# Kernel tuning notes

Measured on AMD Instinct MI355X. Metric: run time of the kernel, lower is better.

Reference implementation:

```python
import jax, jax.numpy as jnp
import numpy as np

VOXEL = 0.1      # voxel_size[0] == voxel_size[1]
OUT_FACTOR = 8
PC_MIN = -51.2   # pc_range[0] == pc_range[1]
OVERLAP = 0.2    # gaussian_overlap
MIN_RADIUS = 2
FH = FW = 128    # 1024 // 8


def gaussian_radius(height, width, min_overlap):
    # mmdet3d / CenterPoint formula, vectorized; returns min(r1, r2, r3)
    b1 = height + width
    c1 = width * height * (1.0 - min_overlap) / (1.0 + min_overlap)
    sq1 = jnp.sqrt(jnp.maximum(b1 * b1 - 4.0 * c1, 0.0))
    r1 = (b1 + sq1) / 2.0

    b2 = 2.0 * (height + width)
    c2 = (1.0 - min_overlap) * width * height
    sq2 = jnp.sqrt(jnp.maximum(b2 * b2 - 16.0 * c2, 0.0))
    r2 = (b2 + sq2) / 2.0

    a3 = 4.0 * min_overlap
    b3 = -2.0 * min_overlap * (height + width)
    c3 = (min_overlap - 1.0) * width * height
    sq3 = jnp.sqrt(jnp.maximum(b3 * b3 - 4.0 * a3 * c3, 0.0))
    r3 = (b3 + sq3) / 2.0
    return jnp.minimum(jnp.minimum(r1, r2), r3)


def setup_inputs() -> dict:
    key = jax.random.key(0)
    k1, k2, k3, k4 = jax.random.split(key, 4)
    B, N = 4, 1024
    xy = jax.random.uniform(k1, (B, N, 2), minval=-51.2, maxval=51.2)
    wl = jax.random.uniform(k2, (B, N, 2), minval=0.5, maxval=6.0)   # box dx, dy in meters
    rest = jax.random.normal(k3, (B, N, 3))
    # box layout: [x, y, z, w(dx), l(dy), h, yaw]
    boxes = jnp.concatenate([xy, rest[..., :1], wl, rest[..., 1:]], axis=-1)
    scores = jax.random.uniform(k4, (B, N))
    return {"boxes": boxes, "scores": scores, "batch_size": 4}


def _generate_mask(boxes, scores):
    scale = VOXEL * OUT_FACTOR  # 0.8 m per feature-map pixel
    w_fm = boxes[..., 3] / scale                      # (B, N)
    l_fm = boxes[..., 4] / scale
    valid = (w_fm > 0) & (l_fm > 0) & (w_fm <= 1000.0) & (l_fm <= 1000.0)

    r = gaussian_radius(l_fm, w_fm, OVERLAP)          # (length_fm, width_fm) order as in source
    r = jnp.where(valid, r, float(MIN_RADIUS))
    radius = jnp.maximum(MIN_RADIUS, jnp.floor(r).astype(jnp.int32))  # int(radius.item())

    # int(coor.item()) truncates toward zero; astype(int32) matches for the in-bounds range
    cx = ((boxes[..., 0] - PC_MIN) / scale).astype(jnp.int32)         # (B, N)
    cy = ((boxes[..., 1] - PC_MIN) / scale).astype(jnp.int32)
    valid = valid & (cx >= 0) & (cx < FW) & (cy >= 0) & (cy < FH)

    sigma = (2.0 * radius.astype(jnp.float32) + 1.0) / 6.0            # (B, N)

    xs = jnp.arange(FW, dtype=jnp.int32)
    ys = jnp.arange(FH, dtype=jnp.int32)
    dx = xs[None, None, :] - cx[..., None]            # (B, N, FW)
    dy = ys[None, None, :] - cy[..., None]            # (B, N, FH)

    d2 = (dy.astype(jnp.float32)[..., :, None] ** 2
          + dx.astype(jnp.float32)[..., None, :] ** 2)                # (B, N, FH, FW)
    g = jnp.exp(-d2 / (2.0 * sigma ** 2)[..., None, None])
    eps = jnp.finfo(jnp.float32).eps                   # gaussian_2d zeroes values < eps * max (max == 1)
    g = jnp.where(g < eps, 0.0, g)

    # clip stamp to the (2r+1)x(2r+1) window around the center, as draw_heatmap_gaussian does
    win = ((jnp.abs(dy) <= radius[..., None])[..., :, None]
           & (jnp.abs(dx) <= radius[..., None])[..., None, :])        # (B, N, FH, FW)
    g = jnp.where(win & valid[..., None, None], g * scores[..., None, None], 0.0)

    heat = jnp.max(g, axis=1)                          # max-accumulate over boxes; init mask is zeros
    return heat[:, None, :, :]                         # (B, 1, FH, FW)


def reference(boxes, scores, batch_size):
    return _generate_mask(boxes, scores)
```

## Files before the change

### kernel.cpp

```cpp
#include <hip/hip_runtime.h>

#define FH 128
#define FW 128
#define MIN_RADIUS 2

__global__ void __launch_bounds__(64)
stamp_gaussians(const float* __restrict__ boxes,
                const float* __restrict__ scores,
                float* __restrict__ out,
                int N) {
    const int box = blockIdx.x;
    const int b   = box / N;

    const float* bx = boxes + (size_t)box * 7;
    const float x = bx[0];
    const float y = bx[1];
    const float w = bx[3];
    const float l = bx[4];

    const float scale = 0.8f;
    const float w_fm = w / scale;
    const float l_fm = l / scale;

    bool valid = (w_fm > 0.0f) && (l_fm > 0.0f) &&
                 (w_fm <= 1000.0f) && (l_fm <= 1000.0f);

    const float h  = l_fm;
    const float wd = w_fm;
    const float ov = 0.2f;

    const float b1  = h + wd;
    const float c1  = wd * h * (1.0f - ov) / (1.0f + ov);
    const float sq1 = sqrtf(fmaxf(b1 * b1 - 4.0f * c1, 0.0f));
    const float r1  = (b1 + sq1) * 0.5f;

    const float b2  = 2.0f * (h + wd);
    const float c2  = (1.0f - ov) * wd * h;
    const float sq2 = sqrtf(fmaxf(b2 * b2 - 16.0f * c2, 0.0f));
    const float r2  = (b2 + sq2) * 0.5f;

    const float a3  = 4.0f * ov;
    const float b3  = -2.0f * ov * (h + wd);
    const float c3  = (ov - 1.0f) * wd * h;
    const float sq3 = sqrtf(fmaxf(b3 * b3 - 4.0f * a3 * c3, 0.0f));
    const float r3  = (b3 + sq3) * 0.5f;

    float r = fminf(fminf(r1, r2), r3);
    if (!valid) r = (float)MIN_RADIUS;
    const int radius = max(MIN_RADIUS, (int)floorf(r));

    const int cx = (int)((x - (-51.2f)) / scale);
    const int cy = (int)((y - (-51.2f)) / scale);
    valid = valid && (cx >= 0) && (cx < FW) && (cy >= 0) && (cy < FH);
    if (!valid) return;

    const float sigma   = (2.0f * (float)radius + 1.0f) / 6.0f;
    const float denom   = 2.0f * sigma * sigma;
    const float score   = scores[box];
    const float eps     = 1.1920928955078125e-07f;

    const int W    = 2 * radius + 1;
    const int npix = W * W;
    float* outb = out + (size_t)b * FH * FW;

    for (int p = threadIdx.x; p < npix; p += blockDim.x) {
        const int oy = p / W - radius;
        const int ox = p % W - radius;
        const int gy = cy + oy;
        const int gx = cx + ox;
        if (gy < 0 || gy >= FH || gx < 0 || gx >= FW) continue;

        const float d2 = (float)(oy * oy + ox * ox);
        float g = expf(-d2 / denom);
        if (g < eps) g = 0.0f;
        const float val = g * score;
        if (val > 0.0f) {
            atomicMax((unsigned int*)&outb[gy * FW + gx], __float_as_uint(val));
        }
    }
}

extern "C" void kernel_launch(void* const* d_in, const int* in_sizes, int n_in,
                              void* d_out, int out_size, void* d_ws, size_t ws_size,
                              hipStream_t stream) {
    const float* boxes  = (const float*)d_in[0];
    const float* scores = (const float*)d_in[1];
    float* out = (float*)d_out;

    const int B = out_size / (FH * FW);
    const int N = in_sizes[1] / B;

    hipMemsetAsync(d_out, 0, (size_t)out_size * sizeof(float), stream);

    stamp_gaussians<<<B * N, 64, 0, stream>>>(boxes, scores, out, N);
}
```

Before: 13.72 us.

## Replace per-box atomic scatter with per-tile gather over culled boxes

The kernel now launches one block per 32x8 output tile instead of one block per box scattering with atomicMax. Each block recomputes every box's radius, keeps in shared memory only the boxes whose window overlaps the tile, and then each thread computes its pixel's max directly. This removes the global atomics and the separate memset launch. In exchange every tile redundantly recomputes all N box radii and relies on N <= 1024 for the shared-memory buffers.

```diff
diff --git a/kernel.cpp b/kernel.cpp
--- a/kernel.cpp
+++ b/kernel.cpp
@@ -2,82 +2,110 @@
 
 #define FH 128
 #define FW 128
+#define TW 32
+#define TH 8
+#define TILES_X (FW / TW)
+#define TILES_Y (FH / TH)
+#define TILES_PER_IMG (TILES_X * TILES_Y)
+#define MAXN 1024
 #define MIN_RADIUS 2
 
-__global__ void __launch_bounds__(64)
-stamp_gaussians(const float* __restrict__ boxes,
-                const float* __restrict__ scores,
-                float* __restrict__ out,
-                int N) {
-    const int box = blockIdx.x;
-    const int b   = box / N;
+__global__ void __launch_bounds__(256)
+mask_gather(const float* __restrict__ boxes,
+            const float* __restrict__ scores,
+            float* __restrict__ out,
+            int N) {
+    __shared__ int   s_cnt;
+    __shared__ int   s_pack[MAXN];
+    __shared__ float s_score[MAXN];
+    __shared__ float s_ninv[MAXN];
 
-    const float* bx = boxes + (size_t)box * 7;
-    const float x = bx[0];
-    const float y = bx[1];
-    const float w = bx[3];
-    const float l = bx[4];
+    const int blk = blockIdx.x;
+    const int b   = blk / TILES_PER_IMG;
+    const int t   = blk % TILES_PER_IMG;
+    const int x0  = (t % TILES_X) * TW;
+    const int y0  = (t / TILES_X) * TH;
+    const int tid = threadIdx.x;
 
-    const float scale = 0.8f;
-    const float w_fm = w / scale;
-    const float l_fm = l / scale;
+    if (tid == 0) s_cnt = 0;
+    __syncthreads();
 
-    bool valid = (w_fm > 0.0f) && (l_fm > 0.0f) &&
-                 (w_fm <= 1000.0f) && (l_fm <= 1000.0f);
+    for (int n = tid; n < N; n += 256) {
+        const float* bx = boxes + (size_t)(b * N + n) * 7;
+        const float x = bx[0];
+        const float y = bx[1];
+        const float w = bx[3];
+        const float l = bx[4];
 
-    const float h  = l_fm;
-    const float wd = w_fm;
-    const float ov = 0.2f;
+        const float scale = 0.8f;
+        const float w_fm = w / scale;
+        const float l_fm = l / scale;
 
-    const float b1  = h + wd;
-    const float c1  = wd * h * (1.0f - ov) / (1.0f + ov);
-    const float sq1 = sqrtf(fmaxf(b1 * b1 - 4.0f * c1, 0.0f));
-    const float r1  = (b1 + sq1) * 0.5f;
+        bool valid = (w_fm > 0.0f) && (l_fm > 0.0f) &&
+                     (w_fm <= 1000.0f) && (l_fm <= 1000.0f);
 
-    const float b2  = 2.0f * (h + wd);
-    const float c2  = (1.0f - ov) * wd * h;
-    const float sq2 = sqrtf(fmaxf(b2 * b2 - 16.0f * c2, 0.0f));
-    const float r2  = (b2 + sq2) * 0.5f;
+        const float h  = l_fm;
+        const float wd = w_fm;
+        const float ov = 0.2f;
 
-    const float a3  = 4.0f * ov;
-    const float b3  = -2.0f * ov * (h + wd);
-    const float c3  = (ov - 1.0f) * wd * h;
-    const float sq3 = sqrtf(fmaxf(b3 * b3 - 4.0f * a3 * c3, 0.0f));
-    const float r3  = (b3 + sq3) * 0.5f;
+        const float b1  = h + wd;
+        const float c1  = wd * h * (1.0f - ov) / (1.0f + ov);
+        const float r1  = (b1 + sqrtf(fmaxf(b1 * b1 - 4.0f * c1, 0.0f))) * 0.5f;
 
-    float r = fminf(fminf(r1, r2), r3);
-    if (!valid) r = (float)MIN_RADIUS;
-    const int radius = max(MIN_RADIUS, (int)floorf(r));
+        const float b2  = 2.0f * (h + wd);
+        const float c2  = (1.0f - ov) * wd * h;
+        const float r2  = (b2 + sqrtf(fmaxf(b2 * b2 - 16.0f * c2, 0.0f))) * 0.5f;
 
-    const int cx = (int)((x - (-51.2f)) / scale);
-    const int cy = (int)((y - (-51.2f)) / scale);
-    valid = valid && (cx >= 0) && (cx < FW) && (cy >= 0) && (cy < FH);
-    if (!valid) return;
+        const float a3  = 4.0f * ov;
+        const float b3  = -2.0f * ov * (h + wd);
+        const float c3  = (ov - 1.0f) * wd * h;
+        const float r3  = (b3 + sqrtf(fmaxf(b3 * b3 - 4.0f * a3 * c3, 0.0f))) * 0.5f;
 
-    const float sigma   = (2.0f * (float)radius + 1.0f) / 6.0f;
-    const float denom   = 2.0f * sigma * sigma;
-    const float score   = scores[box];
-    const float eps     = 1.1920928955078125e-07f;
+        float r = fminf(fminf(r1, r2), r3);
+        if (!valid) r = (float)MIN_RADIUS;
+        const int radius = max(MIN_RADIUS, (int)floorf(r));
 
-    const int W    = 2 * radius + 1;
-    const int npix = W * W;
-    float* outb = out + (size_t)b * FH * FW;
+        const int cx = (int)((x + 51.2f) / scale);
+        const int cy = (int)((y + 51.2f) / scale);
+        valid = valid && (cx >= 0) && (cx < FW) && (cy >= 0) && (cy < FH);
 
-    for (int p = threadIdx.x; p < npix; p += blockDim.x) {
-        const int oy = p / W - radius;
-        const int ox = p % W - radius;
-        const int gy = cy + oy;
-        const int gx = cx + ox;
-        if (gy < 0 || gy >= FH || gx < 0 || gx >= FW) continue;
+        const bool overlap = valid &&
+            (cx + radius >= x0) && (cx - radius <= x0 + TW - 1) &&
+            (cy + radius >= y0) && (cy - radius <= y0 + TH - 1);
 
-        const float d2 = (float)(oy * oy + ox * ox);
-        float g = expf(-d2 / denom);
-        if (g < eps) g = 0.0f;
-        const float val = g * score;
-        if (val > 0.0f) {
-            atomicMax((unsigned int*)&outb[gy * FW + gx], __float_as_uint(val));
+        if (overlap) {
+            const float sigma = (2.0f * (float)radius + 1.0f) / 6.0f;
+            const float denom = 2.0f * sigma * sigma;
+            const int slot = atomicAdd(&s_cnt, 1);
+            s_pack[slot]  = cx | (cy << 8) | (radius << 16);
+            s_score[slot] = scores[b * N + n];
+            s_ninv[slot]  = -1.0f / denom;
         }
     }
+    __syncthreads();
+
+    const int px = x0 + (tid & (TW - 1));
+    const int py = y0 + (tid / TW);
+    const int cnt = s_cnt;
+    const float eps = 1.1920928955078125e-07f;
+
+    float m = 0.0f;
+    for (int i = 0; i < cnt; ++i) {
+        const int p  = s_pack[i];
+        const int cx = p & 0xff;
+        const int cy = (p >> 8) & 0xff;
+        const int r  = p >> 16;
+        const int dx = px - cx;
+        const int dy = py - cy;
+        if (abs(dx) <= r && abs(dy) <= r) {
+            const float d2 = (float)(dx * dx + dy * dy);
+            float g = expf(d2 * s_ninv[i]);
+            if (g < eps) g = 0.0f;
+            m = fmaxf(m, g * s_score[i]);
+        }
+    }
+
+    out[(size_t)b * FH * FW + py * FW + px] = m;
 }
 
 extern "C" void kernel_launch(void* const* d_in, const int* in_sizes, int n_in,
@@ -90,7 +118,5 @@
     const int B = out_size / (FH * FW);
     const int N = in_sizes[1] / B;
 
-    hipMemsetAsync(d_out, 0, (size_t)out_size * sizeof(float), stream);
-
-    stamp_gaussians<<<B * N, 64, 0, stream>>>(boxes, scores, out, N);
+    mask_gather<<<B * TILES_PER_IMG, 256, 0, stream>>>(boxes, scores, out, N);
 }
```

Measured after the change: 14.13 us. +3.0%, slower.
